# Kernel tuning notes

Hardware: AMD Instinct MI355X
Metric: run time of the kernel (lower is better)

## Reference

```python
import jax, jax.numpy as jnp
import numpy as np


def _avgpool(x, k):
    # x: [B, C, H, W] -> [B, C, H//k, W//k] via non-overlapping mean pooling
    B, C, H, W = x.shape
    return x.reshape(B, C, H // k, k, W // k, k).mean(axis=(3, 5))


def _multiscale_tokens(x):
    # concat flattened pooled maps along token dim: [B, C, sum_k (H/k)*(W/k)]
    B, C, H, W = x.shape
    parts = [_avgpool(x, k).reshape(B, C, -1) for k in (16, 8, 4, 2)]
    return jnp.concatenate(parts, axis=2)


def setup_inputs() -> dict:
    key = jax.random.key(0)
    x = jax.random.normal(key, (16, 256, 128, 128), dtype=jnp.float32)
    gamma = jnp.zeros((1,), dtype=jnp.float32)
    return {"x": x, "gamma": gamma}


def reference(x, gamma):
    B, C, H, W = x.shape
    # q and k pooling are identical in the original module (recomputed redundantly)
    tokens = _multiscale_tokens(x)                      # [B, C, T]
    energy = jnp.einsum('bct,bdt->bcd', tokens, tokens)  # [B, C, C]
    energy_new = jnp.max(energy, axis=-1, keepdims=True) - energy
    attention = jax.nn.softmax(energy_new, axis=-1)      # [B, C, C]
    proj_value = x.reshape(B, C, H * W)                  # [B, C, HW]
    out = jnp.einsum('bcd,bdn->bcn', attention, proj_value).reshape(B, C, H, W)
    return gamma * out + x
```

## Files before the change

### kernel.cpp

```cpp
#include <hip/hip_runtime.h>
#include <hip/hip_bf16.h>

#define B_  16
#define C_  256
#define W_  128
#define HW_ 16384
#define T_  5440
#define NSPLIT 17

typedef __bf16 bf16;
typedef __bf16 bf16x2 __attribute__((ext_vector_type(2)));
typedef __bf16 bf16x4 __attribute__((ext_vector_type(4)));
typedef __bf16 bf16x8 __attribute__((ext_vector_type(8)));
typedef float  f32x4  __attribute__((ext_vector_type(4)));

__global__ __launch_bounds__(256) void pool_kernel(const float* __restrict__ x,
                                                   bf16* __restrict__ tokens) {
    __shared__ float s2[64 * 64];
    __shared__ float s4[32 * 32];
    __shared__ float s8[16 * 16];
    const int blk = blockIdx.x;
    const float* plane = x + ((size_t)blk << 14);
    bf16* tok = tokens + (size_t)blk * T_;
    const int tid = threadIdx.x;

    for (int it = 0; it < 8; ++it) {
        int task = it * 256 + tid;
        int i  = task >> 5;
        int jp = task & 31;
        const float4 r0 = *(const float4*)(plane + (2 * i) * W_ + 4 * jp);
        const float4 r1 = *(const float4*)(plane + (2 * i + 1) * W_ + 4 * jp);
        float p0 = (r0.x + r0.y + r1.x + r1.y) * 0.25f;
        float p1 = (r0.z + r0.w + r1.z + r1.w) * 0.25f;
        s2[i * 64 + 2 * jp]     = p0;
        s2[i * 64 + 2 * jp + 1] = p1;
        bf16x2 w; w.x = (bf16)p0; w.y = (bf16)p1;
        *(bf16x2*)(tok + 1344 + i * 64 + 2 * jp) = w;
    }
    __syncthreads();
    for (int it = 0; it < 4; ++it) {
        int task = it * 256 + tid;
        int i = task >> 5, j = task & 31;
        float v = 0.25f * (s2[(2 * i) * 64 + 2 * j] + s2[(2 * i) * 64 + 2 * j + 1] +
                           s2[(2 * i + 1) * 64 + 2 * j] + s2[(2 * i + 1) * 64 + 2 * j + 1]);
        s4[i * 32 + j] = v;
        tok[320 + i * 32 + j] = (bf16)v;
    }
    __syncthreads();
    {
        int i = tid >> 4, j = tid & 15;
        float v = 0.25f * (s4[(2 * i) * 32 + 2 * j] + s4[(2 * i) * 32 + 2 * j + 1] +
                           s4[(2 * i + 1) * 32 + 2 * j] + s4[(2 * i + 1) * 32 + 2 * j + 1]);
        s8[i * 16 + j] = v;
        tok[64 + tid] = (bf16)v;
    }
    __syncthreads();
    if (tid < 64) {
        int i = tid >> 3, j = tid & 7;
        float v = 0.25f * (s8[(2 * i) * 16 + 2 * j] + s8[(2 * i) * 16 + 2 * j + 1] +
                           s8[(2 * i + 1) * 16 + 2 * j] + s8[(2 * i + 1) * 16 + 2 * j + 1]);
        tok[tid] = (bf16)v;
    }
}

__global__ __launch_bounds__(256) void energy_kernel(const bf16* __restrict__ tokens,
                                                     float* __restrict__ part) {
    __shared__ bf16 As[128 * 40];
    __shared__ bf16 Bs[128 * 40];
    const int blk  = blockIdx.x;
    const int s    = blk >> 6;
    const int rem  = blk & 63;
    const int b    = rem >> 2;
    const int tile = rem & 3;
    const int cm0  = (tile >> 1) << 7;
    const int cn0  = (tile & 1) << 7;
    const int kbase = s * (T_ / NSPLIT);
    const int tid  = threadIdx.x;
    const int lane = tid & 63;
    const int w    = tid >> 6;
    const int wm = (w >> 1) * 64, wn = (w & 1) * 64;
    const int lm = lane & 15;
    const int q8 = (lane >> 4) * 8;
    f32x4 acc[4][4] = {};
    for (int ki = 0; ki < (T_ / NSPLIT) / 32; ++ki) {
        const int k0 = kbase + ki * 32;
        __syncthreads();
        for (int it = 0; it < 2; ++it) {
            int slot = it * 256 + tid;
            int r   = slot >> 2;
            int c8  = (slot & 3) * 8;
            *(int4*)(As + r * 40 + c8) = *(const int4*)(tokens + (size_t)(b * C_ + cm0 + r) * T_ + k0 + c8);
            *(int4*)(Bs + r * 40 + c8) = *(const int4*)(tokens + (size_t)(b * C_ + cn0 + r) * T_ + k0 + c8);
        }
        __syncthreads();
        bf16x8 af[4], bfr[4];
        for (int mi = 0; mi < 4; ++mi)
            af[mi] = *(const bf16x8*)(As + (wm + mi * 16 + lm) * 40 + q8);
        for (int ni = 0; ni < 4; ++ni)
            bfr[ni] = *(const bf16x8*)(Bs + (wn + ni * 16 + lm) * 40 + q8);
        for (int mi = 0; mi < 4; ++mi)
            for (int ni = 0; ni < 4; ++ni)
                acc[mi][ni] = __builtin_amdgcn_mfma_f32_16x16x32_bf16(af[mi], bfr[ni], acc[mi][ni], 0, 0, 0);
    }
    float* P = part + ((size_t)(s * 4096 + b * C_) << 8);
    const int row0 = (lane >> 4) * 4;
    for (int mi = 0; mi < 4; ++mi)
        for (int ni = 0; ni < 4; ++ni) {
            f32x4 v = acc[mi][ni];
            int row = cm0 + wm + mi * 16 + row0;
            int col = cn0 + wn + ni * 16 + lm;
            for (int e = 0; e < 4; ++e)
                P[((size_t)(row + e) << 8) + col] = v[e];
        }
}

__global__ __launch_bounds__(256) void softmax_kernel(const float* __restrict__ part,
                                                      bf16* __restrict__ att) {
    const int row  = blockIdx.x * 4 + (threadIdx.x >> 6);
    const int lane = threadIdx.x & 63;
    float4 e = {0.f, 0.f, 0.f, 0.f};
    for (int s = 0; s < NSPLIT; ++s) {
        const float4 p = *(const float4*)(part + ((size_t)(s * 4096 + row) << 8) + lane * 4);
        e.x += p.x; e.y += p.y; e.z += p.z; e.w += p.w;
    }
    float mn = fminf(fminf(e.x, e.y), fminf(e.z, e.w));
    for (int off = 32; off > 0; off >>= 1) mn = fminf(mn, __shfl_xor(mn, off));
    float p0 = __expf(mn - e.x), p1 = __expf(mn - e.y);
    float p2 = __expf(mn - e.z), p3 = __expf(mn - e.w);
    float s = p0 + p1 + p2 + p3;
    for (int off = 32; off > 0; off >>= 1) s += __shfl_xor(s, off);
    float inv = 1.0f / s;
    bf16x4 o;
    o.x = (bf16)(p0 * inv); o.y = (bf16)(p1 * inv);
    o.z = (bf16)(p2 * inv); o.w = (bf16)(p3 * inv);
    *(bf16x4*)(att + ((size_t)row << 8) + lane * 4) = o;
}

__global__ __launch_bounds__(256, 2) void out_kernel(const bf16* __restrict__ att,
                                                     const float* __restrict__ x,
                                                     const float* __restrict__ gamma,
                                                     float* __restrict__ out) {
    __shared__ __align__(16) char smem[33792];
    bf16* As = (bf16*)smem;
    bf16* Bs = (bf16*)(smem + 20480);
    const int b  = blockIdx.x >> 7;
    const int n0 = (blockIdx.x & 127) << 7;
    const int tid  = threadIdx.x;
    const int lane = tid & 63;
    const int w    = tid >> 6;
    const int wm   = w * 64;
    const int lm = lane & 15;
    const int q4 = lane >> 4;
    const int q8 = q4 * 8;
    const float g = gamma[0];
    const bf16*  attb = att + ((size_t)b << 16);
    const float* xb   = x + ((size_t)b << 22);
    f32x4 acc[4][8] = {};
    for (int kk = 0; kk < 8; ++kk) {
        const int k0 = kk * 32;
        __syncthreads();
        for (int it = 0; it < 4; ++it) {
            int slot = it * 256 + tid;
            int r  = slot >> 2;
            int c8 = (slot & 3) * 8;
            *(int4*)(As + r * 40 + c8) = *(const int4*)(attb + ((size_t)r << 8) + k0 + c8);
        }
        for (int it = 0; it < 4; ++it) {
            int slot = it * 256 + tid;
            int r  = slot >> 5;
            int cg = slot & 31;
            float4 v = *(const float4*)(xb + ((size_t)(k0 + r) << 14) + n0 + cg * 4);
            int nn = cg * 4;
            Bs[(nn + 0) * 40 + r] = (bf16)v.x;
            Bs[(nn + 1) * 40 + r] = (bf16)v.y;
            Bs[(nn + 2) * 40 + r] = (bf16)v.z;
            Bs[(nn + 3) * 40 + r] = (bf16)v.w;
        }
        __syncthreads();
        bf16x8 af[4], bfr[8];
        for (int mi = 0; mi < 4; ++mi)
            af[mi] = *(const bf16x8*)(As + (wm + mi * 16 + lm) * 40 + q8);
        for (int ni = 0; ni < 8; ++ni)
            bfr[ni] = *(const bf16x8*)(Bs + (ni * 16 + lm) * 40 + q8);
        for (int mi = 0; mi < 4; ++mi)
            for (int ni = 0; ni < 8; ++ni)
                acc[mi][ni] = __builtin_amdgcn_mfma_f32_16x16x32_bf16(af[mi], bfr[ni], acc[mi][ni], 0, 0, 0);
    }
    float* buf = (float*)(smem + w * 8448);
    __syncthreads();
    for (int mi = 0; mi < 4; ++mi) {
        for (int ni = 0; ni < 8; ++ni) {
            f32x4 v = acc[mi][ni];
            int c = ni * 16 + lm;
            buf[(q4 * 4 + 0) * 132 + c] = v.x;
            buf[(q4 * 4 + 1) * 132 + c] = v.y;
            buf[(q4 * 4 + 2) * 132 + c] = v.z;
            buf[(q4 * 4 + 3) * 132 + c] = v.w;
        }
        __syncthreads();
        for (int t = 0; t < 8; ++t) {
            int idx = t * 64 + lane;
            int r  = idx >> 5;
            int c4 = (idx & 31) * 4;
            f32x4 pv = *(const f32x4*)(buf + r * 132 + c4);
            int c = wm + mi * 16 + r;
            size_t gi = ((size_t)b << 22) + ((size_t)c << 14) + n0 + c4;
            float4 xv = *(const float4*)(x + gi);
            float4 o;
            o.x = g * pv.x + xv.x;
            o.y = g * pv.y + xv.y;
            o.z = g * pv.z + xv.z;
            o.w = g * pv.w + xv.w;
            *(float4*)(out + gi) = o;
        }
        __syncthreads();
    }
}

__global__ __launch_bounds__(256) void fallback_copy(const float* __restrict__ x,
                                                     const float* __restrict__ gamma,
                                                     float* __restrict__ out, size_t n) {
    size_t i = (size_t)blockIdx.x * 256 + threadIdx.x;
    size_t stride = (size_t)gridDim.x * 256;
    float g = gamma[0];
    for (; i < n; i += stride) out[i] = x[i] + g * 0.0f;
}

extern "C" void kernel_launch(void* const* d_in, const int* in_sizes, int n_in,
                              void* d_out, int out_size, void* d_ws, size_t ws_size,
                              hipStream_t stream) {
    const float* x     = (const float*)d_in[0];
    const float* gamma = (const float*)d_in[1];
    float* out = (float*)d_out;

    const size_t ATT_BYTES = (size_t)B_ * C_ * C_ * 2;
    if (ws_size < ATT_BYTES) {
        size_t n = (size_t)B_ * C_ * HW_;
        fallback_copy<<<2048, 256, 0, stream>>>(x, gamma, out, n);
        return;
    }
    bf16*  tokens = (bf16*)d_out;
    float* part   = (float*)((char*)d_out + ((size_t)64 << 20));
    bf16*  att    = (bf16*)d_ws;

    pool_kernel<<<dim3(B_ * C_), dim3(256), 0, stream>>>(x, tokens);
    energy_kernel<<<dim3(NSPLIT * B_ * 4), dim3(256), 0, stream>>>(tokens, part);
    softmax_kernel<<<dim3(B_ * C_ / 4), dim3(256), 0, stream>>>(part, att);
    out_kernel<<<dim3(B_ * 128), dim3(256), 0, stream>>>(att, x, gamma, out);
}
```

Measured before the change: 602.1 us.

## Prefetch x tiles into registers and stream attention via global_load_lds in out GEMM

```diff
diff --git a/kernel.cpp b/kernel.cpp
--- a/kernel.cpp
+++ b/kernel.cpp
@@ -6,13 +6,23 @@
 #define W_  128
 #define HW_ 16384
 #define T_  5440
-#define NSPLIT 17
+#define NSPLIT 10
 
 typedef __bf16 bf16;
 typedef __bf16 bf16x2 __attribute__((ext_vector_type(2)));
 typedef __bf16 bf16x4 __attribute__((ext_vector_type(4)));
 typedef __bf16 bf16x8 __attribute__((ext_vector_type(8)));
 typedef float  f32x4  __attribute__((ext_vector_type(4)));
+
+__device__ __forceinline__ void gload_lds16(const void* g, void* l) {
+    __builtin_amdgcn_global_load_lds(
+        (const __attribute__((address_space(1))) void*)g,
+        (__attribute__((address_space(3))) void*)l, 16, 0, 0);
+}
+
+__device__ __forceinline__ int bs_addr(int n, int q4) {
+    return (n & 3) * 2048 + q4 * 512 + (((n >> 2) ^ (q4 << 1)) & 31) * 16;
+}
 
 __global__ __launch_bounds__(256) void pool_kernel(const float* __restrict__ x,
                                                    bf16* __restrict__ tokens) {
@@ -34,8 +44,8 @@
         float p1 = (r0.z + r0.w + r1.z + r1.w) * 0.25f;
         s2[i * 64 + 2 * jp]     = p0;
         s2[i * 64 + 2 * jp + 1] = p1;
-        bf16x2 w; w.x = (bf16)p0; w.y = (bf16)p1;
-        *(bf16x2*)(tok + 1344 + i * 64 + 2 * jp) = w;
+        bf16x2 wv; wv.x = (bf16)p0; wv.y = (bf16)p1;
+        *(bf16x2*)(tok + 1344 + i * 64 + 2 * jp) = wv;
     }
     __syncthreads();
     for (int it = 0; it < 4; ++it) {
@@ -141,8 +151,8 @@
                                                      const float* __restrict__ gamma,
                                                      float* __restrict__ out) {
     __shared__ __align__(16) char smem[33792];
-    bf16* As = (bf16*)smem;
-    bf16* Bs = (bf16*)(smem + 20480);
+    bf16* As  = (bf16*)smem;
+    char* BsB = smem + 16384;
     const int b  = blockIdx.x >> 7;
     const int n0 = (blockIdx.x & 127) << 7;
     const int tid  = threadIdx.x;
@@ -153,51 +163,70 @@
     const int q4 = lane >> 4;
     const int q8 = q4 * 8;
     const float g = gamma[0];
-    const bf16*  attb = att + ((size_t)b << 16);
-    const float* xb   = x + ((size_t)b << 22);
+    const bf16* attb = att + ((size_t)b << 16);
+    const int cg = tid & 31;
+    const int kq = tid >> 5;
+    const float* xsrc = x + ((size_t)b << 22) + ((size_t)(kq * 4) << 14) + n0 + cg * 4;
+
     f32x4 acc[4][8] = {};
+    f32x4 vj[4];
+    #pragma unroll
+    for (int j = 0; j < 4; ++j) vj[j] = *(const f32x4*)(xsrc + ((size_t)j << 14));
+
     for (int kk = 0; kk < 8; ++kk) {
         const int k0 = kk * 32;
         __syncthreads();
+        #pragma unroll
         for (int it = 0; it < 4; ++it) {
-            int slot = it * 256 + tid;
+            int slot = it * 256 + w * 64 + lane;
             int r  = slot >> 2;
             int c8 = (slot & 3) * 8;
-            *(int4*)(As + r * 40 + c8) = *(const int4*)(attb + ((size_t)r << 8) + k0 + c8);
-        }
-        for (int it = 0; it < 4; ++it) {
-            int slot = it * 256 + tid;
-            int r  = slot >> 5;
-            int cg = slot & 31;
-            float4 v = *(const float4*)(xb + ((size_t)(k0 + r) << 14) + n0 + cg * 4);
-            int nn = cg * 4;
-            Bs[(nn + 0) * 40 + r] = (bf16)v.x;
-            Bs[(nn + 1) * 40 + r] = (bf16)v.y;
-            Bs[(nn + 2) * 40 + r] = (bf16)v.z;
-            Bs[(nn + 3) * 40 + r] = (bf16)v.w;
-        }
-        __syncthreads();
-        bf16x8 af[4], bfr[8];
+            gload_lds16(attb + ((size_t)r << 8) + k0 + c8,
+                        As + (size_t)(it * 256 + w * 64) * 8);
+        }
+        {
+            const int gq = kq >> 1;
+            const int h  = (kq & 1) * 8;
+            #pragma unroll
+            for (int e = 0; e < 4; ++e) {
+                bf16x4 wv;
+                wv.x = (bf16)vj[0][e]; wv.y = (bf16)vj[1][e];
+                wv.z = (bf16)vj[2][e]; wv.w = (bf16)vj[3][e];
+                *(bf16x4*)(BsB + bs_addr(cg * 4 + e, gq) + h) = wv;
+            }
+        }
+        __syncthreads();
+        if (kk < 7) {
+            const float* xs2 = xsrc + ((size_t)(kk + 1) << 19);
+            #pragma unroll
+            for (int j = 0; j < 4; ++j) vj[j] = *(const f32x4*)(xs2 + ((size_t)j << 14));
+        }
+        bf16x8 af[4];
+        #pragma unroll
         for (int mi = 0; mi < 4; ++mi)
-            af[mi] = *(const bf16x8*)(As + (wm + mi * 16 + lm) * 40 + q8);
-        for (int ni = 0; ni < 8; ++ni)
-            bfr[ni] = *(const bf16x8*)(Bs + (ni * 16 + lm) * 40 + q8);
-        for (int mi = 0; mi < 4; ++mi)
-            for (int ni = 0; ni < 8; ++ni)
-                acc[mi][ni] = __builtin_amdgcn_mfma_f32_16x16x32_bf16(af[mi], bfr[ni], acc[mi][ni], 0, 0, 0);
+            af[mi] = *(const bf16x8*)(As + (wm + mi * 16 + lm) * 32 + q8);
+        #pragma unroll
+        for (int ni = 0; ni < 8; ++ni) {
+            bf16x8 bfr = *(const bf16x8*)(BsB + bs_addr(ni * 16 + lm, q4));
+            #pragma unroll
+            for (int mi = 0; mi < 4; ++mi)
+                acc[mi][ni] = __builtin_amdgcn_mfma_f32_16x16x32_bf16(af[mi], bfr, acc[mi][ni], 0, 0, 0);
+        }
     }
     float* buf = (float*)(smem + w * 8448);
     __syncthreads();
     for (int mi = 0; mi < 4; ++mi) {
+        #pragma unroll
         for (int ni = 0; ni < 8; ++ni) {
             f32x4 v = acc[mi][ni];
             int c = ni * 16 + lm;
-            buf[(q4 * 4 + 0) * 132 + c] = v.x;
-            buf[(q4 * 4 + 1) * 132 + c] = v.y;
-            buf[(q4 * 4 + 2) * 132 + c] = v.z;
-            buf[(q4 * 4 + 3) * 132 + c] = v.w;
-        }
-        __syncthreads();
+            buf[(q4 * 4 + 0) * 132 + c] = v[0];
+            buf[(q4 * 4 + 1) * 132 + c] = v[1];
+            buf[(q4 * 4 + 2) * 132 + c] = v[2];
+            buf[(q4 * 4 + 3) * 132 + c] = v[3];
+        }
+        __syncthreads();
+        #pragma unroll
         for (int t = 0; t < 8; ++t) {
             int idx = t * 64 + lane;
             int r  = idx >> 5;
@@ -207,10 +236,10 @@
             size_t gi = ((size_t)b << 22) + ((size_t)c << 14) + n0 + c4;
             float4 xv = *(const float4*)(x + gi);
             float4 o;
-            o.x = g * pv.x + xv.x;
-            o.y = g * pv.y + xv.y;
-            o.z = g * pv.z + xv.z;
-            o.w = g * pv.w + xv.w;
+            o.x = g * pv[0] + xv.x;
+            o.y = g * pv[1] + xv.y;
+            o.z = g * pv[2] + xv.z;
+            o.w = g * pv[3] + xv.w;
             *(float4*)(out + gi) = o;
         }
         __syncthreads();
```

Measured after the change: 586.5 us. -2.6%, faster.
